# Kernel tuning notes

Measured on AMD Instinct MI355X. Metric: run time of the kernel, lower is better.

Reference implementation:

```python
import jax, jax.numpy as jnp
import numpy as np

B, S, H, F, E, TOPK = 4, 2048, 1024, 3584, 8, 2
W_SCALE = 0.02  # keep router logits / activations numerically sane


def setup_inputs() -> dict:
    key = jax.random.key(0)
    k1, k2, k3, k4, k5 = jax.random.split(key, 5)
    return {
        "hidden_states": jax.random.normal(k1, (B, S, H), dtype=jnp.float32),
        "gate_w": jax.random.normal(k2, (E, H), dtype=jnp.float32) * W_SCALE,
        "w1": jax.random.normal(k3, (E, F, H), dtype=jnp.float32) * W_SCALE,
        "w2": jax.random.normal(k4, (E, H, F), dtype=jnp.float32) * W_SCALE,
        "w3": jax.random.normal(k5, (E, F, H), dtype=jnp.float32) * W_SCALE,
        "top_k": TOPK,
    }


def reference(hidden_states, gate_w, w1, w2, w3, top_k):
    b, s, h = hidden_states.shape
    x = hidden_states.reshape(-1, h)                       # [T, H]
    router_logits = x @ gate_w.T                           # [T, E]
    probs = jax.nn.softmax(router_logits.astype(jnp.float32), axis=-1)
    routing_weights, selected_experts = jax.lax.top_k(probs, top_k)  # [T, k]
    routing_weights = routing_weights / routing_weights.sum(axis=-1, keepdims=True)
    routing_weights = routing_weights.astype(x.dtype)
    n_experts = gate_w.shape[0]
    # combine weights: [T, E], zero for unselected experts
    combine = (jax.nn.one_hot(selected_experts, n_experts, dtype=routing_weights.dtype)
               * routing_weights[..., None]).sum(axis=1)
    out = jnp.zeros_like(x)
    for e in range(n_experts):
        hgate = jax.nn.silu(x @ w1[e].T) * (x @ w3[e].T)   # [T, F]
        out = out + (hgate @ w2[e].T) * combine[:, e:e + 1]
    return out.reshape(b, s, h), router_logits
```

## Files before the change

### kernel.cpp

```cpp
#include <hip/hip_runtime.h>
#include <hip/hip_bf16.h>
#include <stdint.h>

#define T_TOK 8192
#define H_DIM 1024
#define F_DIM 3584
#define E_NUM 8

#define BM 128
#define BN 128
#define BK 32
#define LDT 40

typedef __attribute__((ext_vector_type(8))) short bf16x8;
typedef __attribute__((ext_vector_type(4))) float f32x4;

__device__ __forceinline__ short f2bf(float f) {
    union { float f; uint32_t u; } v; v.f = f;
    uint32_t r = v.u + 0x7fffu + ((v.u >> 16) & 1u);
    return (short)(r >> 16);
}

__device__ __forceinline__ uint32_t pack_bf16x2(float a, float b) {
    union { float f; uint32_t u; } ua, ub;
    ua.f = a; ub.f = b;
    return __builtin_amdgcn_perm(ub.u + 0x8000u, ua.u + 0x8000u, 0x07060302u);
}

__device__ __forceinline__ void cvt_store16(const f32x4* v, short* dst) {
    uint32_t w[8];
    #pragma unroll
    for (int i = 0; i < 4; i++) {
        w[2*i]   = pack_bf16x2(v[i][0], v[i][1]);
        w[2*i+1] = pack_bf16x2(v[i][2], v[i][3]);
    }
    ((uint32_t*)dst)[0] = w[0]; ((uint32_t*)dst)[1] = w[1];
    ((uint32_t*)dst)[2] = w[2]; ((uint32_t*)dst)[3] = w[3];
    ((uint32_t*)dst)[4] = w[4]; ((uint32_t*)dst)[5] = w[5];
    ((uint32_t*)dst)[6] = w[6]; ((uint32_t*)dst)[7] = w[7];
}

__device__ __forceinline__ void zero16_store(short* dst) {
    bf16x8 z;
    #pragma unroll
    for (int i = 0; i < 8; i++) z[i] = 0;
    *(bf16x8*)dst = z;
    *((bf16x8*)dst + 1) = z;
}

__device__ __forceinline__ void load16(f32x4* dst, const float* __restrict__ src) {
    const f32x4* p = (const f32x4*)src;
    #pragma unroll
    for (int i = 0; i < 4; i++) dst[i] = p[i];
}

__global__ void router_kernel(const float* __restrict__ x,
                              const float* __restrict__ gate_w,
                              float* __restrict__ logits_out,
                              int* __restrict__ counts,
                              int* __restrict__ lists,
                              float* __restrict__ wgt) {
    int wave = (blockIdx.x * blockDim.x + threadIdx.x) >> 6;
    int lane = threadIdx.x & 63;
    if (wave >= T_TOK) return;
    const float* xr = x + (size_t)wave * H_DIM;

    float acc[E_NUM];
    #pragma unroll
    for (int e = 0; e < E_NUM; e++) acc[e] = 0.f;

    for (int i = lane; i < H_DIM; i += 64) {
        float xv = xr[i];
        #pragma unroll
        for (int e = 0; e < E_NUM; e++) acc[e] += xv * gate_w[e * H_DIM + i];
    }
    #pragma unroll
    for (int off = 32; off > 0; off >>= 1) {
        #pragma unroll
        for (int e = 0; e < E_NUM; e++) acc[e] += __shfl_xor(acc[e], off);
    }

    if (lane == 0) {
        int t = wave;
        #pragma unroll
        for (int e = 0; e < E_NUM; e++) logits_out[t * E_NUM + e] = acc[e];
        int i0 = 0; float v0 = acc[0];
        #pragma unroll
        for (int e = 1; e < E_NUM; e++) if (acc[e] > v0) { v0 = acc[e]; i0 = e; }
        int i1 = -1; float v1 = -1e30f;
        #pragma unroll
        for (int e = 0; e < E_NUM; e++) if (e != i0 && acc[e] > v1) { v1 = acc[e]; i1 = e; }
        float e1 = __expf(v1 - v0);
        float inv = 1.f / (1.f + e1);
        int a0 = 2 * t, a1 = 2 * t + 1;
        wgt[a0] = inv;
        wgt[a1] = e1 * inv;
        int p0 = atomicAdd(&counts[i0], 1);
        lists[i0 * T_TOK + p0] = a0;
        int p1 = atomicAdd(&counts[i1], 1);
        lists[i1 * T_TOK + p1] = a1;
    }
}

__global__ __launch_bounds__(256, 2)
void gemm1_kernel(const float* __restrict__ x,
                  const float* __restrict__ w1,
                  const float* __restrict__ w3,
                  const int* __restrict__ counts,
                  const int* __restrict__ lists,
                  unsigned short* __restrict__ hgate) {
    const int e = blockIdx.z;
    const int count = counts[e];
    const int mbase = blockIdx.y * BM;
    if (mbase >= count) return;
    const int nbase = blockIdx.x * BN;

    __shared__ short As[BM * LDT];
    __shared__ short B1s[BN * LDT];
    __shared__ short B3s[BN * LDT];

    const int tid = threadIdx.x;
    const int r = tid >> 1;
    const int half = tid & 1;

    const float* arow = nullptr;
    {
        int m = mbase + r;
        if (m < count) {
            int a = lists[e * T_TOK + m];
            arow = x + (size_t)(a >> 1) * H_DIM;
        }
    }
    const float* b1row = w1 + ((size_t)e * F_DIM + (nbase + r)) * H_DIM;
    const float* b3row = w3 + ((size_t)e * F_DIM + (nbase + r)) * H_DIM;

    const int lane = tid & 63;
    const int wid = tid >> 6;
    const int wm = wid >> 1, wn = wid & 1;
    const int lr = lane & 15, lq = lane >> 4;

    f32x4 acc1[4][4], acc3[4][4];
    #pragma unroll
    for (int i = 0; i < 4; i++)
        #pragma unroll
        for (int j = 0; j < 4; j++) {
            acc1[i][j] = (f32x4){0.f, 0.f, 0.f, 0.f};
            acc3[i][j] = (f32x4){0.f, 0.f, 0.f, 0.f};
        }

    f32x4 ap[4], b1p[4], b3p[4];
    {
        const int koff = half * 16;
        if (arow) load16(ap, arow + koff);
        load16(b1p, b1row + koff);
        load16(b3p, b3row + koff);
    }

    short* adst  = &As[r * LDT + half * 16];
    short* b1dst = &B1s[r * LDT + half * 16];
    short* b3dst = &B3s[r * LDT + half * 16];

    for (int k0 = 0; k0 < H_DIM; k0 += BK) {
        if (arow) cvt_store16(ap, adst); else zero16_store(adst);
        cvt_store16(b1p, b1dst);
        cvt_store16(b3p, b3dst);
        __syncthreads();

        int kn = k0 + BK;
        if (kn < H_DIM) {
            const int koff = kn + half * 16;
            if (arow) load16(ap, arow + koff);
            load16(b1p, b1row + koff);
            load16(b3p, b3row + koff);
        }

        bf16x8 af[4], b1f[4], b3f[4];
        #pragma unroll
        for (int i = 0; i < 4; i++)
            af[i] = *(const bf16x8*)&As[(wm * 64 + i * 16 + lr) * LDT + lq * 8];
        #pragma unroll
        for (int j = 0; j < 4; j++) {
            b1f[j] = *(const bf16x8*)&B1s[(wn * 64 + j * 16 + lr) * LDT + lq * 8];
            b3f[j] = *(const bf16x8*)&B3s[(wn * 64 + j * 16 + lr) * LDT + lq * 8];
        }
        #pragma unroll
        for (int i = 0; i < 4; i++)
            #pragma unroll
            for (int j = 0; j < 4; j++) {
                acc1[i][j] = __builtin_amdgcn_mfma_f32_16x16x32_bf16(af[i], b1f[j], acc1[i][j], 0, 0, 0);
                acc3[i][j] = __builtin_amdgcn_mfma_f32_16x16x32_bf16(af[i], b3f[j], acc3[i][j], 0, 0, 0);
            }
        __syncthreads();
    }

    #pragma unroll
    for (int i = 0; i < 4; i++) {
        #pragma unroll
        for (int rg = 0; rg < 4; rg++) {
            int mm = mbase + wm * 64 + i * 16 + lq * 4 + rg;
            if (mm >= count) continue;
            int a = lists[e * T_TOK + mm];
            unsigned short* hrow = hgate + (size_t)a * F_DIM + nbase;
            #pragma unroll
            for (int j = 0; j < 4; j++) {
                float g = acc1[i][j][rg];
                float u = acc3[i][j][rg];
                float s = (g / (1.f + __expf(-g))) * u;
                hrow[wn * 64 + j * 16 + lr] = (unsigned short)f2bf(s);
            }
        }
    }
}

__global__ __launch_bounds__(256, 2)
void gemm2_kernel(const unsigned short* __restrict__ hgate,
                  const float* __restrict__ w2,
                  const int* __restrict__ counts,
                  const int* __restrict__ lists,
                  const float* __restrict__ wgt,
                  float* __restrict__ out) {
    const int e = blockIdx.z;
    const int count = counts[e];
    const int mbase = blockIdx.y * BM;
    if (mbase >= count) return;
    const int nbase = blockIdx.x * BN;

    __shared__ short As[BM * LDT];
    __shared__ short Bs[BN * LDT];

    const int tid = threadIdx.x;
    const int r = tid >> 1;
    const int half = tid & 1;

    const unsigned short* arow = nullptr;
    {
        int m = mbase + r;
        if (m < count) {
            int a = lists[e * T_TOK + m];
            arow = hgate + (size_t)a * F_DIM;
        }
    }
    const float* brow = w2 + ((size_t)e * H_DIM + (nbase + r)) * F_DIM;

    const int lane = tid & 63;
    const int wid = tid >> 6;
    const int wm = wid >> 1, wn = wid & 1;
    const int lr = lane & 15, lq = lane >> 4;

    f32x4 acc[4][4];
    #pragma unroll
    for (int i = 0; i < 4; i++)
        #pragma unroll
        for (int j = 0; j < 4; j++) acc[i][j] = (f32x4){0.f, 0.f, 0.f, 0.f};

    bf16x8 a2p[2];
    f32x4 bp[4];
    {
        const int koff = half * 16;
        if (arow) {
            const bf16x8* p = (const bf16x8*)(arow + koff);
            a2p[0] = p[0]; a2p[1] = p[1];
        }
        load16(bp, brow + koff);
    }

    short* adst = &As[r * LDT + half * 16];
    short* bdst = &Bs[r * LDT + half * 16];

    for (int k0 = 0; k0 < F_DIM; k0 += BK) {
        if (arow) {
            *(bf16x8*)adst = a2p[0];
            *((bf16x8*)adst + 1) = a2p[1];
        } else {
            zero16_store(adst);
        }
        cvt_store16(bp, bdst);
        __syncthreads();

        int kn = k0 + BK;
        if (kn < F_DIM) {
            const int koff = kn + half * 16;
            if (arow) {
                const bf16x8* p = (const bf16x8*)(arow + koff);
                a2p[0] = p[0]; a2p[1] = p[1];
            }
            load16(bp, brow + koff);
        }

        bf16x8 af[4], bf[4];
        #pragma unroll
        for (int i = 0; i < 4; i++)
            af[i] = *(const bf16x8*)&As[(wm * 64 + i * 16 + lr) * LDT + lq * 8];
        #pragma unroll
        for (int j = 0; j < 4; j++)
            bf[j] = *(const bf16x8*)&Bs[(wn * 64 + j * 16 + lr) * LDT + lq * 8];
        #pragma unroll
        for (int i = 0; i < 4; i++)
            #pragma unroll
            for (int j = 0; j < 4; j++)
                acc[i][j] = __builtin_amdgcn_mfma_f32_16x16x32_bf16(af[i], bf[j], acc[i][j], 0, 0, 0);
        __syncthreads();
    }

    #pragma unroll
    for (int i = 0; i < 4; i++) {
        #pragma unroll
        for (int rg = 0; rg < 4; rg++) {
            int mm = mbase + wm * 64 + i * 16 + lq * 4 + rg;
            if (mm >= count) continue;
            int a = lists[e * T_TOK + mm];
            float w = wgt[a];
            int t = a >> 1;
            float* orow = out + (size_t)t * H_DIM + nbase;
            #pragma unroll
            for (int j = 0; j < 4; j++)
                atomicAdd(&orow[wn * 64 + j * 16 + lr], acc[i][j][rg] * w);
        }
    }
}

extern "C" void kernel_launch(void* const* d_in, const int* in_sizes, int n_in,
                              void* d_out, int out_size, void* d_ws, size_t ws_size,
                              hipStream_t stream) {
    const float* x      = (const float*)d_in[0];
    const float* gate_w = (const float*)d_in[1];
    const float* w1     = (const float*)d_in[2];
    const float* w2     = (const float*)d_in[3];
    const float* w3     = (const float*)d_in[4];

    float* out    = (float*)d_out;
    float* logits = out + (size_t)T_TOK * H_DIM;

    char* ws = (char*)d_ws;
    int*   counts = (int*)(ws + 0);
    int*   lists  = (int*)(ws + 1024);
    float* wgt    = (float*)(ws + 1024 + (size_t)E_NUM * T_TOK * 4);
    unsigned short* hgate =
        (unsigned short*)(ws + 1024 + (size_t)E_NUM * T_TOK * 4 + (size_t)T_TOK * 2 * 4);

    hipMemsetAsync(counts, 0, E_NUM * sizeof(int), stream);
    hipMemsetAsync(out, 0, (size_t)T_TOK * H_DIM * sizeof(float), stream);

    router_kernel<<<T_TOK / 4, 256, 0, stream>>>(x, gate_w, logits, counts, lists, wgt);

    gemm1_kernel<<<dim3(F_DIM / BN, T_TOK / BM, E_NUM), 256, 0, stream>>>(
        x, w1, w3, counts, lists, hgate);

    gemm2_kernel<<<dim3(H_DIM / BN, T_TOK / BM, E_NUM), 256, 0, stream>>>(
        hgate, w2, counts, lists, wgt, out);
}
```

Measured before the change: 1.231 ms.

## Pre-convert operands to bf16 and stream tiles directly into double-buffered LDS

```diff
diff --git a/kernel.cpp b/kernel.cpp
--- a/kernel.cpp
+++ b/kernel.cpp
@@ -1,5 +1,4 @@
 #include <hip/hip_runtime.h>
-#include <hip/hip_bf16.h>
 #include <stdint.h>
 
 #define T_TOK 8192
@@ -10,10 +9,16 @@
 #define BM 128
 #define BN 128
 #define BK 32
-#define LDT 40
 
 typedef __attribute__((ext_vector_type(8))) short bf16x8;
 typedef __attribute__((ext_vector_type(4))) float f32x4;
+typedef __attribute__((ext_vector_type(4))) uint32_t u32x4;
+
+typedef const __attribute__((address_space(1))) void gv_t;
+typedef __attribute__((address_space(3))) void lv_t;
+
+#define GLOAD_LDS16(g, l) \
+    __builtin_amdgcn_global_load_lds((gv_t*)(g), (lv_t*)(l), 16, 0, 0)
 
 __device__ __forceinline__ short f2bf(float f) {
     union { float f; uint32_t u; } v; v.f = f;
@@ -27,31 +32,30 @@
     return __builtin_amdgcn_perm(ub.u + 0x8000u, ua.u + 0x8000u, 0x07060302u);
 }
 
-__device__ __forceinline__ void cvt_store16(const f32x4* v, short* dst) {
-    uint32_t w[8];
-    #pragma unroll
-    for (int i = 0; i < 4; i++) {
-        w[2*i]   = pack_bf16x2(v[i][0], v[i][1]);
-        w[2*i+1] = pack_bf16x2(v[i][2], v[i][3]);
-    }
-    ((uint32_t*)dst)[0] = w[0]; ((uint32_t*)dst)[1] = w[1];
-    ((uint32_t*)dst)[2] = w[2]; ((uint32_t*)dst)[3] = w[3];
-    ((uint32_t*)dst)[4] = w[4]; ((uint32_t*)dst)[5] = w[5];
-    ((uint32_t*)dst)[6] = w[6]; ((uint32_t*)dst)[7] = w[7];
-}
-
-__device__ __forceinline__ void zero16_store(short* dst) {
-    bf16x8 z;
-    #pragma unroll
-    for (int i = 0; i < 8; i++) z[i] = 0;
-    *(bf16x8*)dst = z;
-    *((bf16x8*)dst + 1) = z;
-}
-
-__device__ __forceinline__ void load16(f32x4* dst, const float* __restrict__ src) {
-    const f32x4* p = (const f32x4*)src;
-    #pragma unroll
-    for (int i = 0; i < 4; i++) dst[i] = p[i];
+__global__ __launch_bounds__(256)
+void cvt4_kernel(const float* __restrict__ w1, const float* __restrict__ w3,
+                 const float* __restrict__ w2, const float* __restrict__ x,
+                 unsigned short* __restrict__ w1b, unsigned short* __restrict__ w3b,
+                 unsigned short* __restrict__ w2b, unsigned short* __restrict__ xb) {
+    const int z = blockIdx.z;
+    const float* src; unsigned short* dst; int n8;
+    if (z == 0)      { src = w1; dst = w1b; n8 = (E_NUM * F_DIM * H_DIM) / 8; }
+    else if (z == 1) { src = w3; dst = w3b; n8 = (E_NUM * F_DIM * H_DIM) / 8; }
+    else if (z == 2) { src = w2; dst = w2b; n8 = (E_NUM * H_DIM * F_DIM) / 8; }
+    else             { src = x;  dst = xb;  n8 = (T_TOK * H_DIM) / 8; }
+
+    int idx = blockIdx.x * blockDim.x + threadIdx.x;
+    int stride = gridDim.x * blockDim.x;
+    for (int i = idx; i < n8; i += stride) {
+        const f32x4* p = (const f32x4*)src + (size_t)i * 2;
+        f32x4 v0 = p[0], v1 = p[1];
+        u32x4 w;
+        w[0] = pack_bf16x2(v0[0], v0[1]);
+        w[1] = pack_bf16x2(v0[2], v0[3]);
+        w[2] = pack_bf16x2(v1[0], v1[1]);
+        w[3] = pack_bf16x2(v1[2], v1[3]);
+        ((u32x4*)dst)[i] = w;
+    }
 }
 
 __global__ void router_kernel(const float* __restrict__ x,
@@ -103,9 +107,9 @@
 }
 
 __global__ __launch_bounds__(256, 2)
-void gemm1_kernel(const float* __restrict__ x,
-                  const float* __restrict__ w1,
-                  const float* __restrict__ w3,
+void gemm1_kernel(const unsigned short* __restrict__ xb,
+                  const unsigned short* __restrict__ w1b,
+                  const unsigned short* __restrict__ w3b,
                   const int* __restrict__ counts,
                   const int* __restrict__ lists,
                   unsigned short* __restrict__ hgate) {
@@ -115,30 +119,46 @@
     if (mbase >= count) return;
     const int nbase = blockIdx.x * BN;
 
-    __shared__ short As[BM * LDT];
-    __shared__ short B1s[BN * LDT];
-    __shared__ short B3s[BN * LDT];
+    __shared__ short As[2][BM * BK];
+    __shared__ short B1s[2][BM * BK];
+    __shared__ short B3s[2][BM * BK];
 
     const int tid = threadIdx.x;
-    const int r = tid >> 1;
-    const int half = tid & 1;
-
-    const float* arow = nullptr;
-    {
-        int m = mbase + r;
-        if (m < count) {
-            int a = lists[e * T_TOK + m];
-            arow = x + (size_t)(a >> 1) * H_DIM;
-        }
-    }
-    const float* b1row = w1 + ((size_t)e * F_DIM + (nbase + r)) * H_DIM;
-    const float* b3row = w3 + ((size_t)e * F_DIM + (nbase + r)) * H_DIM;
-
     const int lane = tid & 63;
     const int wid = tid >> 6;
     const int wm = wid >> 1, wn = wid & 1;
     const int lr = lane & 15, lq = lane >> 4;
 
+    const int srow0 = wid * 32 + (lane >> 2);
+    const int srow1 = srow0 + 16;
+    const int kp8 = (lane & 3) * 8;
+
+    const unsigned short *ag0, *ag1;
+    {
+        int m0 = mbase + srow0; if (m0 >= count) m0 = count - 1;
+        int m1 = mbase + srow1; if (m1 >= count) m1 = count - 1;
+        ag0 = xb + (size_t)(lists[e * T_TOK + m0] >> 1) * H_DIM + kp8;
+        ag1 = xb + (size_t)(lists[e * T_TOK + m1] >> 1) * H_DIM + kp8;
+    }
+    const unsigned short* b1g0 = w1b + ((size_t)e * F_DIM + nbase + srow0) * H_DIM + kp8;
+    const unsigned short* b1g1 = b1g0 + (size_t)16 * H_DIM;
+    const unsigned short* b3g0 = w3b + ((size_t)e * F_DIM + nbase + srow0) * H_DIM + kp8;
+    const unsigned short* b3g1 = b3g0 + (size_t)16 * H_DIM;
+
+    const int ldsc = wid * 1024;
+
+    auto stage = [&](int buf) {
+        GLOAD_LDS16(ag0,  &As[buf][ldsc]);
+        GLOAD_LDS16(ag1,  &As[buf][ldsc + 512]);
+        GLOAD_LDS16(b1g0, &B1s[buf][ldsc]);
+        GLOAD_LDS16(b1g1, &B1s[buf][ldsc + 512]);
+        GLOAD_LDS16(b3g0, &B3s[buf][ldsc]);
+        GLOAD_LDS16(b3g1, &B3s[buf][ldsc + 512]);
+        ag0 += BK; ag1 += BK;
+        b1g0 += BK; b1g1 += BK;
+        b3g0 += BK; b3g1 += BK;
+    };
+
     f32x4 acc1[4][4], acc3[4][4];
     #pragma unroll
     for (int i = 0; i < 4; i++)
@@ -148,40 +168,22 @@
             acc3[i][j] = (f32x4){0.f, 0.f, 0.f, 0.f};
         }
 
-    f32x4 ap[4], b1p[4], b3p[4];
-    {
-        const int koff = half * 16;
-        if (arow) load16(ap, arow + koff);
-        load16(b1p, b1row + koff);
-        load16(b3p, b3row + koff);
-    }
-
-    short* adst  = &As[r * LDT + half * 16];
-    short* b1dst = &B1s[r * LDT + half * 16];
-    short* b3dst = &B3s[r * LDT + half * 16];
-
-    for (int k0 = 0; k0 < H_DIM; k0 += BK) {
-        if (arow) cvt_store16(ap, adst); else zero16_store(adst);
-        cvt_store16(b1p, b1dst);
-        cvt_store16(b3p, b3dst);
-        __syncthreads();
-
-        int kn = k0 + BK;
-        if (kn < H_DIM) {
-            const int koff = kn + half * 16;
-            if (arow) load16(ap, arow + koff);
-            load16(b1p, b1row + koff);
-            load16(b3p, b3row + koff);
-        }
+    stage(0);
+    __syncthreads();
+
+    const int NK = H_DIM / BK;
+    for (int kt = 0; kt < NK; ++kt) {
+        const int cur = kt & 1;
+        if (kt + 1 < NK) stage(cur ^ 1);
 
         bf16x8 af[4], b1f[4], b3f[4];
         #pragma unroll
         for (int i = 0; i < 4; i++)
-            af[i] = *(const bf16x8*)&As[(wm * 64 + i * 16 + lr) * LDT + lq * 8];
+            af[i] = *(const bf16x8*)&As[cur][(wm * 64 + i * 16 + lr) * BK + lq * 8];
         #pragma unroll
         for (int j = 0; j < 4; j++) {
-            b1f[j] = *(const bf16x8*)&B1s[(wn * 64 + j * 16 + lr) * LDT + lq * 8];
-            b3f[j] = *(const bf16x8*)&B3s[(wn * 64 + j * 16 + lr) * LDT + lq * 8];
+            b1f[j] = *(const bf16x8*)&B1s[cur][(wn * 64 + j * 16 + lr) * BK + lq * 8];
+            b3f[j] = *(const bf16x8*)&B3s[cur][(wn * 64 + j * 16 + lr) * BK + lq * 8];
         }
         #pragma unroll
         for (int i = 0; i < 4; i++)
@@ -214,7 +216,7 @@
 
 __global__ __launch_bounds__(256, 2)
 void gemm2_kernel(const unsigned short* __restrict__ hgate,
-                  const float* __restrict__ w2,
+                  const unsigned short* __restrict__ w2b,
                   const int* __restrict__ counts,
                   const int* __restrict__ lists,
                   const float* __restrict__ wgt,
@@ -225,80 +227,66 @@
     if (mbase >= count) return;
     const int nbase = blockIdx.x * BN;
 
-    __shared__ short As[BM * LDT];
-    __shared__ short Bs[BN * LDT];
+    __shared__ short As[2][BM * BK];
+    __shared__ short Bs[2][BM * BK];
 
     const int tid = threadIdx.x;
-    const int r = tid >> 1;
-    const int half = tid & 1;
-
-    const unsigned short* arow = nullptr;
-    {
-        int m = mbase + r;
-        if (m < count) {
-            int a = lists[e * T_TOK + m];
-            arow = hgate + (size_t)a * F_DIM;
-        }
-    }
-    const float* brow = w2 + ((size_t)e * H_DIM + (nbase + r)) * F_DIM;
-
     const int lane = tid & 63;
     const int wid = tid >> 6;
     const int wm = wid >> 1, wn = wid & 1;
     const int lr = lane & 15, lq = lane >> 4;
 
+    const int srow0 = wid * 32 + (lane >> 2);
+    const int srow1 = srow0 + 16;
+    const int kp8 = (lane & 3) * 8;
+
+    const unsigned short *ag0, *ag1;
+    {
+        int m0 = mbase + srow0; if (m0 >= count) m0 = count - 1;
+        int m1 = mbase + srow1; if (m1 >= count) m1 = count - 1;
+        ag0 = hgate + (size_t)lists[e * T_TOK + m0] * F_DIM + kp8;
+        ag1 = hgate + (size_t)lists[e * T_TOK + m1] * F_DIM + kp8;
+    }
+    const unsigned short* bg0 = w2b + ((size_t)e * H_DIM + nbase + srow0) * F_DIM + kp8;
+    const unsigned short* bg1 = bg0 + (size_t)16 * F_DIM;
+
+    const int ldsc = wid * 1024;
+
+    auto stage = [&](int buf) {
+        GLOAD_LDS16(ag0, &As[buf][ldsc]);
+        GLOAD_LDS16(ag1, &As[buf][ldsc + 512]);
+        GLOAD_LDS16(bg0, &Bs[buf][ldsc]);
+        GLOAD_LDS16(bg1, &Bs[buf][ldsc + 512]);
+        ag0 += BK; ag1 += BK;
+        bg0 += BK; bg1 += BK;
+    };
+
     f32x4 acc[4][4];
     #pragma unroll
     for (int i = 0; i < 4; i++)
         #pragma unroll
         for (int j = 0; j < 4; j++) acc[i][j] = (f32x4){0.f, 0.f, 0.f, 0.f};
 
-    bf16x8 a2p[2];
-    f32x4 bp[4];
-    {
-        const int koff = half * 16;
-        if (arow) {
-            const bf16x8* p = (const bf16x8*)(arow + koff);
-            a2p[0] = p[0]; a2p[1] = p[1];
-        }
-        load16(bp, brow + koff);
-    }
-
-    short* adst = &As[r * LDT + half * 16];
-    short* bdst = &Bs[r * LDT + half * 16];
-
-    for (int k0 = 0; k0 < F_DIM; k0 += BK) {
-        if (arow) {
-            *(bf16x8*)adst = a2p[0];
-            *((bf16x8*)adst + 1) = a2p[1];
-        } else {
-            zero16_store(adst);
-        }
-        cvt_store16(bp, bdst);
-        __syncthreads();
-
-        int kn = k0 + BK;
-        if (kn < F_DIM) {
-            const int koff = kn + half * 16;
-            if (arow) {
-                const bf16x8* p = (const bf16x8*)(arow + koff);
-                a2p[0] = p[0]; a2p[1] = p[1];
-            }
-            load16(bp, brow + koff);
-        }
-
-        bf16x8 af[4], bf[4];
+    stage(0);
+    __syncthreads();
+
+    const int NK = F_DIM / BK;
+    for (int kt = 0; kt < NK; ++kt) {
+        const int cur = kt & 1;
+        if (kt + 1 < NK) stage(cur ^ 1);
+
+        bf16x8 af[4], bfr[4];
         #pragma unroll
         for (int i = 0; i < 4; i++)
-            af[i] = *(const bf16x8*)&As[(wm * 64 + i * 16 + lr) * LDT + lq * 8];
+            af[i] = *(const bf16x8*)&As[cur][(wm * 64 + i * 16 + lr) * BK + lq * 8];
         #pragma unroll
         for (int j = 0; j < 4; j++)
-            bf[j] = *(const bf16x8*)&Bs[(wn * 64 + j * 16 + lr) * LDT + lq * 8];
+            bfr[j] = *(const bf16x8*)&Bs[cur][(wn * 64 + j * 16 + lr) * BK + lq * 8];
         #pragma unroll
         for (int i = 0; i < 4; i++)
             #pragma unroll
             for (int j = 0; j < 4; j++)
-                acc[i][j] = __builtin_amdgcn_mfma_f32_16x16x32_bf16(af[i], bf[j], acc[i][j], 0, 0, 0);
+                acc[i][j] = __builtin_amdgcn_mfma_f32_16x16x32_bf16(af[i], bfr[j], acc[i][j], 0, 0, 0);
         __syncthreads();
     }
 
@@ -337,15 +325,21 @@
     float* wgt    = (float*)(ws + 1024 + (size_t)E_NUM * T_TOK * 4);
     unsigned short* hgate =
         (unsigned short*)(ws + 1024 + (size_t)E_NUM * T_TOK * 4 + (size_t)T_TOK * 2 * 4);
+    unsigned short* xb  = hgate + (size_t)2 * T_TOK * F_DIM;
+    unsigned short* w1b = xb + (size_t)T_TOK * H_DIM;
+    unsigned short* w3b = w1b + (size_t)E_NUM * F_DIM * H_DIM;
+    unsigned short* w2b = w3b + (size_t)E_NUM * F_DIM * H_DIM;
 
     hipMemsetAsync(counts, 0, E_NUM * sizeof(int), stream);
     hipMemsetAsync(out, 0, (size_t)T_TOK * H_DIM * sizeof(float), stream);
 
+    cvt4_kernel<<<dim3(1024, 1, 4), 256, 0, stream>>>(w1, w3, w2, x, w1b, w3b, w2b, xb);
+
     router_kernel<<<T_TOK / 4, 256, 0, stream>>>(x, gate_w, logits, counts, lists, wgt);
 
     gemm1_kernel<<<dim3(F_DIM / BN, T_TOK / BM, E_NUM), 256, 0, stream>>>(
-        x, w1, w3, counts, lists, hgate);
+        xb, w1b, w3b, counts, lists, hgate);
 
     gemm2_kernel<<<dim3(H_DIM / BN, T_TOK / BM, E_NUM), 256, 0, stream>>>(
-        hgate, w2, counts, lists, wgt, out);
-}
+        hgate, w2b, counts, lists, wgt, out);
+}
```

Result: faster. 1.157 ms (-6.0%).
